# Kernel optimization log

Measured on AMD Instinct MI355X. Metric: run time of the kernel, lower is better.

Reference implementation:

```python
import jax, jax.numpy as jnp
import numpy as np

N = 100000   # number of nodes
E = 400000   # number of edges
C = 16       # n_in_channels == n_out_channels
L = 16       # node_conv2 .. node_conv17
EPS = 1e-5   # BatchNorm eps


def _bn(h, g, b):
    # training-mode BatchNorm1d over the edge/batch axis (biased variance)
    mu = h.mean(0)
    var = h.var(0)
    return (h - mu) * jax.lax.rsqrt(var + EPS) * g + b


def setup_inputs() -> dict:
    key = jax.random.key(0)
    ks = jax.random.split(key, 6)
    return {
        "edge_features": jax.random.normal(ks[0], (E, C), jnp.float32),
        "edge_index": jax.random.randint(ks[1], (2, E), 0, N),
        "angles": jax.random.normal(ks[2], (E,), jnp.float32),
        "Wn": jax.random.normal(ks[3], (L, C, 2 * C), jnp.float32) / np.sqrt(2.0 * C),
        "bn": jnp.zeros((L, C), jnp.float32),
        "gn": jnp.ones((L, C), jnp.float32),
        "btn": jnp.zeros((L, C), jnp.float32),
        "We": jax.random.normal(ks[4], (C, 2 * C), jnp.float32) / np.sqrt(2.0 * C),
        "be": jnp.zeros((C,), jnp.float32),
        "ge": jnp.ones((C,), jnp.float32),
        "bte": jnp.zeros((C,), jnp.float32),
    }


def _forward(edge_features, edge_index, Wn, bn, gn, btn, We, be, ge, bte):
    src, dst = edge_index[0], edge_index[1]

    # EdgeConvNoNodes: init node features = mean of incident edge features (both endpoints)
    idx = jnp.concatenate([src, dst])                       # [2E]
    feats = jnp.concatenate([edge_features, edge_features], axis=0)
    deg = jax.ops.segment_sum(jnp.ones((2 * E,), edge_features.dtype), idx, N)
    x = jax.ops.segment_sum(feats, idx, N) / jnp.clip(deg, 1.0)[:, None]  # [N, C]

    # in-degree for mean aggregation of the 16 NodeConv1 layers
    deg_in = jnp.clip(jax.ops.segment_sum(jnp.ones((E,), x.dtype), dst, N), 1.0)[:, None]

    def step(x, p):
        W, b, g, bt = p
        # message: Linear(cat(x_i, x_j)) -> BN -> LeakyReLU on [E, C]
        m = jnp.concatenate([x[dst], x[src]], axis=1) @ W.T + b
        m = jax.nn.leaky_relu(_bn(m, g, bt))
        # mean aggregation at target nodes
        return jax.ops.segment_sum(m, dst, N) / deg_in, None

    x, _ = jax.lax.scan(step, x, (Wn, bn, gn, btn))

    # EdgeConv2: per-edge MLP on both edge directions, BN stats shared over [2E]
    pair = jnp.concatenate(
        [jnp.concatenate([x[src], x[dst]], axis=1),
         jnp.concatenate([x[dst], x[src]], axis=1)], axis=0)  # [2E, 2C]
    e = jax.nn.leaky_relu(_bn(pair @ We.T + be, ge, bte))      # [2E, C]
    e_fwd, e_bwd = e[:E], e[E:]
    edge_out = 0.5 * (e_fwd + e_bwd)                           # symmetric edge feature
    side_loss = jnp.mean((e_fwd - e_bwd) ** 2)                 # symmetry side loss
    return edge_out, side_loss


def reference(edge_features, edge_index, angles, Wn, bn, gn, btn, We, be, ge, bte):
    # `angles` is accepted but unused, matching the original forward
    return _forward(edge_features, edge_index, Wn, bn, gn, btn, We, be, ge, bte)
```

## Files before the change

### kernel.cpp

```cpp
#include <hip/hip_runtime.h>
#include <hip/hip_fp16.h>
#include <cstdint>
#include <cstddef>

#define NN 100000
#define EE 400000
#define CC 16
#define LL 16
#define NB 16

typedef unsigned int uint;

__device__ __forceinline__ float lrelu(float v){ return v > 0.0f ? v : 0.01f*v; }

__device__ __forceinline__ float waveSum(float v){
#pragma unroll
  for (int off = 32; off >= 1; off >>= 1) v += __shfl_xor(v, off);
  return v;
}

__device__ __forceinline__ float fma4(float4 w, float4 v, float a){
  a = fmaf(w.x, v.x, a); a = fmaf(w.y, v.y, a);
  a = fmaf(w.z, v.z, a); a = fmaf(w.w, v.w, a);
  return a;
}

__device__ __forceinline__ uint pack_h2(float a, float b){
  __half2 h = __floats2half2_rn(a, b);
  return *reinterpret_cast<uint*>(&h);
}
__device__ __forceinline__ float2 unpack_h2(uint v){
  __half2 h = *reinterpret_cast<__half2*>(&v);
  return __half22float2(h);
}

__global__ __launch_bounds__(256) void k_count(const int* __restrict__ ei,
    int* __restrict__ cdst, int* __restrict__ csrc)
{
  int t = blockIdx.x*256 + threadIdx.x;
  if (t >= EE) return;
  int s = ei[t], d = ei[EE + t];
  atomicAdd(&cdst[d], 1);
  atomicAdd(&csrc[s], 1);
}

__device__ __forceinline__ void scan_one(const int* __restrict__ cnt,
    int* __restrict__ rp, int* __restrict__ bsums, int n, int* sd)
{
  int tid = threadIdx.x;
  int base = blockIdx.x*1024 + tid*4;
  int v0=0,v1=0,v2=0,v3=0;
  if (base+0 < n) v0 = cnt[base+0];
  if (base+1 < n) v1 = cnt[base+1];
  if (base+2 < n) v2 = cnt[base+2];
  if (base+3 < n) v3 = cnt[base+3];
  int tot = v0+v1+v2+v3;
  sd[tid] = tot; __syncthreads();
  for (int off=1; off<256; off<<=1){
    int add = (tid>=off) ? sd[tid-off] : 0;
    __syncthreads();
    sd[tid] += add;
    __syncthreads();
  }
  int excl = sd[tid] - tot;
  if (base+0 < n) rp[base+0] = excl;
  if (base+1 < n) rp[base+1] = excl+v0;
  if (base+2 < n) rp[base+2] = excl+v0+v1;
  if (base+3 < n) rp[base+3] = excl+v0+v1+v2;
  if (tid==255) bsums[blockIdx.x] = sd[255];
  __syncthreads();
}

__global__ __launch_bounds__(256) void k_scan1(const int* __restrict__ ca,
    int* __restrict__ rpa, int* __restrict__ bsa,
    const int* __restrict__ cb, int* __restrict__ rpb, int* __restrict__ bsb, int n)
{
  __shared__ int sd[256];
  scan_one(ca, rpa, bsa, n, sd);
  scan_one(cb, rpb, bsb, n, sd);
}

__device__ __forceinline__ void scan2_one(const int* __restrict__ bsums,
    int* __restrict__ boff, int nseg, int* sd)
{
  int tid = threadIdx.x;
  int v = (tid < nseg) ? bsums[tid] : 0;
  sd[tid] = v; __syncthreads();
  for (int off=1; off<256; off<<=1){
    int add = (tid>=off) ? sd[tid-off] : 0;
    __syncthreads();
    sd[tid] += add;
    __syncthreads();
  }
  if (tid < nseg) boff[tid] = sd[tid] - v;
  __syncthreads();
}

__global__ __launch_bounds__(256) void k_scan2(const int* __restrict__ bsa,
    int* __restrict__ boffa, const int* __restrict__ bsb, int* __restrict__ boffb, int nseg)
{
  __shared__ int sd[256];
  scan2_one(bsa, boffa, nseg, sd);
  scan2_one(bsb, boffb, nseg, sd);
}

__global__ __launch_bounds__(256) void k_scan3(
    int* __restrict__ rpa, int* __restrict__ cura, const int* __restrict__ boffa, int totala,
    int* __restrict__ rpb, int* __restrict__ curb, const int* __restrict__ boffb, int totalb, int n)
{
  int adda = boffa[blockIdx.x];
  int addb = boffb[blockIdx.x];
  int base = blockIdx.x*1024 + threadIdx.x*4;
#pragma unroll
  for (int i=0;i<4;i++){
    if (base+i < n){
      int va = rpa[base+i] + adda; rpa[base+i] = va; cura[base+i] = va;
      int vb = rpb[base+i] + addb; rpb[base+i] = vb; curb[base+i] = vb;
    }
  }
  if (blockIdx.x==0 && threadIdx.x==0){ rpa[n] = totala; rpb[n] = totalb; }
}

__global__ __launch_bounds__(256) void k_fill(const int* __restrict__ ei,
    int* __restrict__ cur, int4* __restrict__ sd4,
    int* __restrict__ curs, int* __restrict__ lsrc)
{
  int t = blockIdx.x*256 + threadIdx.x;
  if (t >= EE) return;
  int s = ei[t], d = ei[EE + t];
  int p = atomicAdd(&cur[d], 1);
  sd4[p] = make_int4(s, d, t, 0);
  int ps = atomicAdd(&curs[s], 1);
  lsrc[ps] = t;
}

__global__ __launch_bounds__(256) void k_gather0(const float* __restrict__ ef,
    const int4* __restrict__ sd4, const int* __restrict__ rp,
    const int* __restrict__ lsrc, const int* __restrict__ rps,
    float* __restrict__ x0, float* __restrict__ invdeg)
{
  int t = blockIdx.x*256 + threadIdx.x;
  if (t >= NN*CC) return;
  int n = t >> 4, c = t & 15;
  int bd = rp[n], ed = rp[n+1];
  int bs = rps[n], es = rps[n+1];
  float acc = 0.0f;
  for (int i=bd; i<ed; i++){
    acc += ef[(size_t)sd4[i].z*CC + c];
  }
  for (int i=bs; i<es; i++){
    acc += ef[(size_t)lsrc[i]*CC + c];
  }
  float dg = fmaxf((float)((ed-bd)+(es-bs)), 1.0f);
  x0[t] = acc / dg;
  if (c == 0){
    invdeg[n] = 1.0f / fmaxf((float)(ed-bd), 1.0f);
  }
}

__global__ __launch_bounds__(256) void k_edge(const float* __restrict__ x,
    const int4* __restrict__ sd4,
    const float* __restrict__ W, const float* __restrict__ b,
    uint* __restrict__ mh, double* __restrict__ st)
{
  __shared__ float sW[512];
  __shared__ float sb16[16];
  __shared__ float sredS[64], sredQ[64];
  for (int i=threadIdx.x; i<512; i+=256) sW[i] = W[i];
  if (threadIdx.x < 16) sb16[threadIdx.x] = b[threadIdx.x];
  __syncthreads();

  int t = blockIdx.x*256 + threadIdx.x;
  bool val = (t < EE);
  float acc[16];
  if (val){
    int4 p = sd4[t];
    const float4* xd4 = (const float4*)(x + (size_t)p.y*CC);
    const float4* xs4 = (const float4*)(x + (size_t)p.x*CC);
    float4 xd0=xd4[0], xd1=xd4[1], xd2=xd4[2], xd3=xd4[3];
    float4 xs0=xs4[0], xs1=xs4[1], xs2=xs4[2], xs3=xs4[3];
#pragma unroll
    for (int c=0;c<16;c++){
      const float4* wr = (const float4*)(sW + c*32);
      float a = sb16[c];
      a = fma4(wr[0],xd0,a); a = fma4(wr[1],xd1,a);
      a = fma4(wr[2],xd2,a); a = fma4(wr[3],xd3,a);
      a = fma4(wr[4],xs0,a); a = fma4(wr[5],xs1,a);
      a = fma4(wr[6],xs2,a); a = fma4(wr[7],xs3,a);
      acc[c] = a;
    }
    uint pk[8];
#pragma unroll
    for (int q=0;q<8;q++) pk[q] = pack_h2(acc[2*q], acc[2*q+1]);
    uint4* po = (uint4*)(mh + (size_t)t*8);
    po[0] = make_uint4(pk[0],pk[1],pk[2],pk[3]);
    po[1] = make_uint4(pk[4],pk[5],pk[6],pk[7]);
  } else {
#pragma unroll
    for (int c=0;c<16;c++) acc[c] = 0.0f;
  }

  int lane = threadIdx.x & 63, w = threadIdx.x >> 6;
#pragma unroll
  for (int c=0;c<16;c++){
    float rs = waveSum(acc[c]);
    float rq = waveSum(acc[c]*acc[c]);
    if (lane == 0){ sredS[w*16+c] = rs; sredQ[w*16+c] = rq; }
  }
  __syncthreads();
  double* stb = st + (size_t)(blockIdx.x & (NB-1))*32;
  if (threadIdx.x < 16){
    int c = threadIdx.x;
    float tot = sredS[c] + sredS[16+c] + sredS[32+c] + sredS[48+c];
    unsafeAtomicAdd(&stb[c], (double)tot);
  } else if (threadIdx.x < 32){
    int c = threadIdx.x - 16;
    float tot = sredQ[c] + sredQ[16+c] + sredQ[32+c] + sredQ[48+c];
    unsafeAtomicAdd(&stb[16+c], (double)tot);
  }
}

__global__ __launch_bounds__(256) void k_node(const uint* __restrict__ mh,
    const int* __restrict__ rp,
    const float* __restrict__ invdeg, const double* __restrict__ st,
    const float* __restrict__ g, const float* __restrict__ bt,
    float* __restrict__ xout)
{
  __shared__ float sA[16], sB[16];
  if (threadIdx.x < 16){
    int c = threadIdx.x;
    double S = 0.0, Q = 0.0;
#pragma unroll
    for (int k=0;k<NB;k++){ S += st[k*32 + c]; Q += st[k*32 + 16 + c]; }
    double mu  = S * (1.0/EE);
    double var = Q * (1.0/EE) - mu*mu;
    float sc = rsqrtf((float)var + 1e-5f);
    float A = sc * g[c];
    sA[c] = A; sB[c] = bt[c] - (float)mu * A;
  }
  __syncthreads();
  int t = blockIdx.x*256 + threadIdx.x;
  int n = t >> 3, cp = t & 7;
  if (n >= NN) return;
  float A0 = sA[2*cp], B0 = sB[2*cp];
  float A1 = sA[2*cp+1], B1 = sB[2*cp+1];
  int beg = rp[n], end = rp[n+1];
  float a0 = 0.0f, a1 = 0.0f;
  for (int i=beg; i<end; i++){
    float2 v = unpack_h2(mh[(size_t)i*8 + cp]);
    a0 += lrelu(fmaf(A0, v.x, B0));
    a1 += lrelu(fmaf(A1, v.y, B1));
  }
  float iv = invdeg[n];
  float2* po = (float2*)(xout + (size_t)n*CC + 2*cp);
  *po = make_float2(a0*iv, a1*iv);
}

__global__ __launch_bounds__(256) void k_uvf(const float* __restrict__ x,
    const float* __restrict__ W, const float* __restrict__ b,
    uint* __restrict__ u, uint* __restrict__ v)
{
  __shared__ float sW[512];
  __shared__ float sb16[16];
  for (int i=threadIdx.x; i<512; i+=256) sW[i] = W[i];
  if (threadIdx.x < 16) sb16[threadIdx.x] = b[threadIdx.x];
  __syncthreads();
  int n = blockIdx.x*256 + threadIdx.x;
  if (n >= NN) return;
  const float4* xr = (const float4*)(x + (size_t)n*CC);
  float4 x0 = xr[0], x1 = xr[1], x2 = xr[2], x3 = xr[3];
  uint up[8], vp[8];
#pragma unroll
  for (int q=0;q<8;q++){
    int c0 = 2*q, c1 = 2*q+1;
    const float4* w0 = (const float4*)(sW + c0*32);
    const float4* w1 = (const float4*)(sW + c1*32);
    float u0 = sb16[c0], u1 = sb16[c1], v0 = 0.f, v1 = 0.f;
    u0 = fma4(w0[0],x0,u0); u0 = fma4(w0[1],x1,u0); u0 = fma4(w0[2],x2,u0); u0 = fma4(w0[3],x3,u0);
    v0 = fma4(w0[4],x0,v0); v0 = fma4(w0[5],x1,v0); v0 = fma4(w0[6],x2,v0); v0 = fma4(w0[7],x3,v0);
    u1 = fma4(w1[0],x0,u1); u1 = fma4(w1[1],x1,u1); u1 = fma4(w1[2],x2,u1); u1 = fma4(w1[3],x3,u1);
    v1 = fma4(w1[4],x0,v1); v1 = fma4(w1[5],x1,v1); v1 = fma4(w1[6],x2,v1); v1 = fma4(w1[7],x3,v1);
    up[q] = pack_h2(u0,u1);
    vp[q] = pack_h2(v0,v1);
  }
  uint4* pu = (uint4*)(u + (size_t)n*8);
  pu[0] = make_uint4(up[0],up[1],up[2],up[3]);
  pu[1] = make_uint4(up[4],up[5],up[6],up[7]);
  uint4* pv = (uint4*)(v + (size_t)n*8);
  pv[0] = make_uint4(vp[0],vp[1],vp[2],vp[3]);
  pv[1] = make_uint4(vp[4],vp[5],vp[6],vp[7]);
}

__global__ __launch_bounds__(256) void k_final1(
    const uint* __restrict__ uf, const uint* __restrict__ vf,
    const int* __restrict__ ei, double* __restrict__ st)
{
  __shared__ float sredS[64], sredQ[64];
  int t = blockIdx.x*256 + threadIdx.x;
  float ls[16], lq[16];
#pragma unroll
  for (int c=0;c<16;c++){ ls[c]=0.f; lq[c]=0.f; }
  if (t < EE){
    int s = ei[t], d = ei[EE+t];
    const uint4* pus = (const uint4*)(uf + (size_t)s*8);
    const uint4* pvd = (const uint4*)(vf + (size_t)d*8);
    const uint4* pud = (const uint4*)(uf + (size_t)d*8);
    const uint4* pvs = (const uint4*)(vf + (size_t)s*8);
    uint4 us0=pus[0], us1=pus[1], vd0=pvd[0], vd1=pvd[1];
    uint4 ud0=pud[0], ud1=pud[1], vs0=pvs[0], vs1=pvs[1];
    uint usw[8]={us0.x,us0.y,us0.z,us0.w, us1.x,us1.y,us1.z,us1.w};
    uint vdw[8]={vd0.x,vd0.y,vd0.z,vd0.w, vd1.x,vd1.y,vd1.z,vd1.w};
    uint udw[8]={ud0.x,ud0.y,ud0.z,ud0.w, ud1.x,ud1.y,ud1.z,ud1.w};
    uint vsw[8]={vs0.x,vs0.y,vs0.z,vs0.w, vs1.x,vs1.y,vs1.z,vs1.w};
#pragma unroll
    for (int q=0;q<8;q++){
      float2 a = unpack_h2(usw[q]), bq = unpack_h2(vdw[q]);
      float2 cc = unpack_h2(udw[q]), dd = unpack_h2(vsw[q]);
      float f0 = a.x + bq.x, f1 = a.y + bq.y;
      float g0 = cc.x + dd.x, g1 = cc.y + dd.y;
      ls[2*q]   += f0 + g0; lq[2*q]   += f0*f0 + g0*g0;
      ls[2*q+1] += f1 + g1; lq[2*q+1] += f1*f1 + g1*g1;
    }
  }
  int lane = threadIdx.x & 63, w = threadIdx.x >> 6;
#pragma unroll
  for (int c=0;c<16;c++){
    float rs = waveSum(ls[c]);
    float rq = waveSum(lq[c]);
    if (lane == 0){ sredS[w*16+c] = rs; sredQ[w*16+c] = rq; }
  }
  __syncthreads();
  double* stb = st + (size_t)(blockIdx.x & (NB-1))*32;
  if (threadIdx.x < 16){
    int c = threadIdx.x;
    float tot = sredS[c] + sredS[16+c] + sredS[32+c] + sredS[48+c];
    unsafeAtomicAdd(&stb[c], (double)tot);
  } else if (threadIdx.x < 32){
    int c = threadIdx.x - 16;
    float tot = sredQ[c] + sredQ[16+c] + sredQ[32+c] + sredQ[48+c];
    unsafeAtomicAdd(&stb[16+c], (double)tot);
  }
}

__global__ __launch_bounds__(256) void k_final2(
    const uint* __restrict__ uf, const uint* __restrict__ vf,
    const int* __restrict__ ei, const double* __restrict__ st,
    const float* __restrict__ g, const float* __restrict__ bt,
    float* __restrict__ out, double* __restrict__ loss)
{
  __shared__ float sA[16], sB[16];
  __shared__ float sl[4];
  if (threadIdx.x < 16){
    int c = threadIdx.x;
    double S = 0.0, Q = 0.0;
#pragma unroll
    for (int k=0;k<NB;k++){ S += st[k*32 + c]; Q += st[k*32 + 16 + c]; }
    double mu  = S * (1.0/(2.0*EE));
    double var = Q * (1.0/(2.0*EE)) - mu*mu;
    float sc = rsqrtf((float)var + 1e-5f);
    float A = sc * g[c];
    sA[c] = A; sB[c] = bt[c] - (float)mu * A;
  }
  __syncthreads();

  int t = blockIdx.x*256 + threadIdx.x;
  float lsum = 0.0f;
  if (t < EE){
    int s = ei[t], d = ei[EE+t];
    const uint4* pus = (const uint4*)(uf + (size_t)s*8);
    const uint4* pvd = (const uint4*)(vf + (size_t)d*8);
    const uint4* pud = (const uint4*)(uf + (size_t)d*8);
    const uint4* pvs = (const uint4*)(vf + (size_t)s*8);
    uint4 us0=pus[0], us1=pus[1], vd0=pvd[0], vd1=pvd[1];
    uint4 ud0=pud[0], ud1=pud[1], vs0=pvs[0], vs1=pvs[1];
    uint usw[8]={us0.x,us0.y,us0.z,us0.w, us1.x,us1.y,us1.z,us1.w};
    uint vdw[8]={vd0.x,vd0.y,vd0.z,vd0.w, vd1.x,vd1.y,vd1.z,vd1.w};
    uint udw[8]={ud0.x,ud0.y,ud0.z,ud0.w, ud1.x,ud1.y,ud1.z,ud1.w};
    uint vsw[8]={vs0.x,vs0.y,vs0.z,vs0.w, vs1.x,vs1.y,vs1.z,vs1.w};
    float fo[16];
#pragma unroll
    for (int q=0;q<8;q++){
      float2 a = unpack_h2(usw[q]), bq = unpack_h2(vdw[q]);
      float2 cc = unpack_h2(udw[q]), dd = unpack_h2(vsw[q]);
      int c0 = 2*q, c1 = 2*q+1;
      float e0 = lrelu(fmaf(sA[c0], a.x + bq.x, sB[c0]));
      float b0 = lrelu(fmaf(sA[c0], cc.x + dd.x, sB[c0]));
      float e1 = lrelu(fmaf(sA[c1], a.y + bq.y, sB[c1]));
      float b1 = lrelu(fmaf(sA[c1], cc.y + dd.y, sB[c1]));
      fo[c0] = 0.5f*(e0 + b0);
      fo[c1] = 0.5f*(e1 + b1);
      float d0 = e0 - b0, d1 = e1 - b1;
      lsum = fmaf(d0, d0, lsum);
      lsum = fmaf(d1, d1, lsum);
    }
    float4* po = (float4*)(out + (size_t)t*CC);
    po[0]=make_float4(fo[0],fo[1],fo[2],fo[3]);
    po[1]=make_float4(fo[4],fo[5],fo[6],fo[7]);
    po[2]=make_float4(fo[8],fo[9],fo[10],fo[11]);
    po[3]=make_float4(fo[12],fo[13],fo[14],fo[15]);
  }
  lsum = waveSum(lsum);
  int lane = threadIdx.x & 63, w = threadIdx.x >> 6;
  if (lane == 0) sl[w] = lsum;
  __syncthreads();
  if (threadIdx.x == 0)
    unsafeAtomicAdd(&loss[blockIdx.x & (NB-1)], (double)(sl[0]+sl[1]+sl[2]+sl[3]));
}

__global__ void k_final3(float* __restrict__ out, const double* __restrict__ loss)
{
  double s = 0.0;
#pragma unroll
  for (int k=0;k<NB;k++) s += loss[k];
  out[(size_t)EE*CC] = (float)(s * (1.0/((double)EE*CC)));
}

extern "C" void kernel_launch(void* const* d_in, const int* in_sizes, int n_in,
                              void* d_out, int out_size, void* d_ws, size_t ws_size,
                              hipStream_t stream)
{
  (void)in_sizes; (void)n_in; (void)out_size; (void)ws_size;
  const float* ef  = (const float*)d_in[0];
  const int*   ei  = (const int*)d_in[1];
  const float* Wn  = (const float*)d_in[3];
  const float* bn  = (const float*)d_in[4];
  const float* gn  = (const float*)d_in[5];
  const float* btn = (const float*)d_in[6];
  const float* We  = (const float*)d_in[7];
  const float* be  = (const float*)d_in[8];
  const float* ge  = (const float*)d_in[9];
  const float* bte = (const float*)d_in[10];
  float* out = (float*)d_out;
  char* ws = (char*)d_ws;

  size_t off = 0;
  auto alloc = [&](size_t bytes)->size_t{
    size_t r = off; off = (off + bytes + 255) & ~(size_t)255; return r;
  };
  size_t o_xa     = alloc((size_t)NN*CC*4);
  size_t o_xb     = alloc((size_t)NN*CC*4);
  size_t o_mh     = alloc((size_t)EE*8*4);
  size_t o_uf     = alloc((size_t)NN*8*4);
  size_t o_vf     = alloc((size_t)NN*8*4);
  size_t o_cdst   = alloc((size_t)NN*4);
  size_t o_csrc   = alloc((size_t)NN*4);
  size_t o_rp     = alloc((size_t)(NN+1)*4);
  size_t o_rps    = alloc((size_t)(NN+1)*4);
  size_t o_cur    = alloc((size_t)NN*4);
  size_t o_curs   = alloc((size_t)NN*4);
  size_t o_sd4    = alloc((size_t)EE*16);
  size_t o_lsrc   = alloc((size_t)EE*4);
  size_t o_bsum   = alloc(512);
  size_t o_bsum2  = alloc(512);
  size_t o_boff   = alloc(512);
  size_t o_boff2  = alloc(512);
  size_t o_stats  = alloc((size_t)(17*NB*32 + NB)*8);
  size_t o_invdeg = alloc((size_t)NN*4);

  float*  x_a     = (float*)(ws + o_xa);
  float*  x_b     = (float*)(ws + o_xb);
  uint*   m_h     = (uint*)(ws + o_mh);
  uint*   u_f     = (uint*)(ws + o_uf);
  uint*   v_f     = (uint*)(ws + o_vf);
  int*    cdst    = (int*)(ws + o_cdst);
  int*    csrc    = (int*)(ws + o_csrc);
  int*    rp      = (int*)(ws + o_rp);
  int*    rps     = (int*)(ws + o_rps);
  int*    cur     = (int*)(ws + o_cur);
  int*    curs    = (int*)(ws + o_curs);
  int4*   sd4     = (int4*)(ws + o_sd4);
  int*    lsrc    = (int*)(ws + o_lsrc);
  int*    bsum    = (int*)(ws + o_bsum);
  int*    bsum2   = (int*)(ws + o_bsum2);
  int*    boff    = (int*)(ws + o_boff);
  int*    boff2   = (int*)(ws + o_boff2);
  double* stats   = (double*)(ws + o_stats);
  double* lossd   = stats + (size_t)17*NB*32;
  float*  invdeg  = (float*)(ws + o_invdeg);

  const int GB_E  = (EE + 255)/256;
  const int GB_NC = (NN*CC + 255)/256;
  const int GB_N8 = (NN*8 + 255)/256;
  const int GB_N  = (NN + 255)/256;
  const int NSEG  = (NN + 1023)/1024;

  hipMemsetAsync(cdst, 0, (size_t)NN*4, stream);
  hipMemsetAsync(csrc, 0, (size_t)NN*4, stream);
  hipMemsetAsync(stats, 0, (size_t)(17*NB*32 + NB)*8, stream);

  k_count<<<GB_E, 256, 0, stream>>>(ei, cdst, csrc);
  k_scan1<<<NSEG, 256, 0, stream>>>(cdst, rp, bsum, csrc, rps, bsum2, NN);
  k_scan2<<<1, 256, 0, stream>>>(bsum, boff, bsum2, boff2, NSEG);
  k_scan3<<<NSEG, 256, 0, stream>>>(rp, cur, boff, EE, rps, curs, boff2, EE, NN);
  k_fill<<<GB_E, 256, 0, stream>>>(ei, cur, sd4, curs, lsrc);
  k_gather0<<<GB_NC, 256, 0, stream>>>(ef, sd4, rp, lsrc, rps, x_a, invdeg);

  const float* xc = x_a;
  float* xn = x_b;
  for (int l = 0; l < LL; ++l){
    double* st = stats + (size_t)l*NB*32;
    const float* Wl = Wn + (size_t)l*CC*2*CC;
    const float* bl = bn + (size_t)l*CC;
    k_edge<<<GB_E, 256, 0, stream>>>(xc, sd4, Wl, bl, m_h, st);
    k_node<<<GB_N8, 256, 0, stream>>>(m_h, rp, invdeg, st,
                                      gn + (size_t)l*CC, btn + (size_t)l*CC, xn);
    float* tmp = (float*)xc; xc = xn; xn = tmp;
  }

  double* stF = stats + (size_t)LL*NB*32;
  k_uvf<<<GB_N, 256, 0, stream>>>(xc, We, be, u_f, v_f);
  k_final1<<<GB_E, 256, 0, stream>>>(u_f, v_f, ei, stF);
  k_final2<<<GB_E, 256, 0, stream>>>(u_f, v_f, ei, stF, ge, bte, out, lossd);
  k_final3<<<1, 1, 0, stream>>>(out, lossd);
}
```

Baseline: 952.0 us.

## Store node features in fp16 and process two edges per thread in k_edge

Node feature buffers switch from fp32 to packed half2, which halves the bytes of every random gather of node rows in the edge and final kernels. k_edge now handles two edges per thread, so each shared-memory weight read feeds two FMAs and the number of wave reductions per edge is halved. k_gather0 moves to one thread per channel pair using float2 loads. Storing node features in fp16 adds rounding error on every one of the 16 layers, and the two-edges-per-thread kernel raises register pressure.

```diff
diff --git a/kernel.cpp b/kernel.cpp
--- a/kernel.cpp
+++ b/kernel.cpp
@@ -19,12 +19,6 @@
   return v;
 }
 
-__device__ __forceinline__ float fma4(float4 w, float4 v, float a){
-  a = fmaf(w.x, v.x, a); a = fmaf(w.y, v.y, a);
-  a = fmaf(w.z, v.z, a); a = fmaf(w.w, v.w, a);
-  return a;
-}
-
 __device__ __forceinline__ uint pack_h2(float a, float b){
   __half2 h = __floats2half2_rn(a, b);
   return *reinterpret_cast<uint*>(&h);
@@ -32,6 +26,14 @@
 __device__ __forceinline__ float2 unpack_h2(uint v){
   __half2 h = *reinterpret_cast<__half2*>(&v);
   return __half22float2(h);
+}
+
+__device__ __forceinline__ void unpack_row(const uint* __restrict__ xh, int n, float* f){
+  const uint4* p = (const uint4*)(xh + (size_t)n*8);
+  uint4 r0 = p[0], r1 = p[1];
+  uint w[8] = {r0.x,r0.y,r0.z,r0.w, r1.x,r1.y,r1.z,r1.w};
+#pragma unroll
+  for (int q=0;q<8;q++){ float2 v = unpack_h2(w[q]); f[2*q]=v.x; f[2*q+1]=v.y; }
 }
 
 __global__ __launch_bounds__(256) void k_count(const int* __restrict__ ei,
@@ -137,28 +139,32 @@
 __global__ __launch_bounds__(256) void k_gather0(const float* __restrict__ ef,
     const int4* __restrict__ sd4, const int* __restrict__ rp,
     const int* __restrict__ lsrc, const int* __restrict__ rps,
-    float* __restrict__ x0, float* __restrict__ invdeg)
-{
-  int t = blockIdx.x*256 + threadIdx.x;
-  if (t >= NN*CC) return;
-  int n = t >> 4, c = t & 15;
+    uint* __restrict__ xh, float* __restrict__ invdeg)
+{
+  int t = blockIdx.x*256 + threadIdx.x;
+  if (t >= NN*8) return;
+  int n = t >> 3, cp = t & 7;
   int bd = rp[n], ed = rp[n+1];
   int bs = rps[n], es = rps[n+1];
-  float acc = 0.0f;
+  float a0 = 0.0f, a1 = 0.0f;
   for (int i=bd; i<ed; i++){
-    acc += ef[(size_t)sd4[i].z*CC + c];
+    const float2* p = (const float2*)(ef + (size_t)sd4[i].z*CC + 2*cp);
+    float2 v = *p;
+    a0 += v.x; a1 += v.y;
   }
   for (int i=bs; i<es; i++){
-    acc += ef[(size_t)lsrc[i]*CC + c];
+    const float2* p = (const float2*)(ef + (size_t)lsrc[i]*CC + 2*cp);
+    float2 v = *p;
+    a0 += v.x; a1 += v.y;
   }
   float dg = fmaxf((float)((ed-bd)+(es-bs)), 1.0f);
-  x0[t] = acc / dg;
-  if (c == 0){
+  xh[(size_t)n*8 + cp] = pack_h2(a0/dg, a1/dg);
+  if (cp == 0){
     invdeg[n] = 1.0f / fmaxf((float)(ed-bd), 1.0f);
   }
 }
 
-__global__ __launch_bounds__(256) void k_edge(const float* __restrict__ x,
+__global__ __launch_bounds__(256) void k_edge(const uint* __restrict__ xh,
     const int4* __restrict__ sd4,
     const float* __restrict__ W, const float* __restrict__ b,
     uint* __restrict__ mh, double* __restrict__ st)
@@ -171,40 +177,51 @@
   __syncthreads();
 
   int t = blockIdx.x*256 + threadIdx.x;
-  bool val = (t < EE);
-  float acc[16];
+  int e0 = 2*t, e1 = 2*t+1;
+  bool val = (e1 < EE);
+  float acc0[16], acc1[16];
   if (val){
-    int4 p = sd4[t];
-    const float4* xd4 = (const float4*)(x + (size_t)p.y*CC);
-    const float4* xs4 = (const float4*)(x + (size_t)p.x*CC);
-    float4 xd0=xd4[0], xd1=xd4[1], xd2=xd4[2], xd3=xd4[3];
-    float4 xs0=xs4[0], xs1=xs4[1], xs2=xs4[2], xs3=xs4[3];
+    int4 p0 = sd4[e0], p1 = sd4[e1];
+    float xa[32], xb[32];
+    unpack_row(xh, p0.y, xa);
+    unpack_row(xh, p0.x, xa + 16);
+    unpack_row(xh, p1.y, xb);
+    unpack_row(xh, p1.x, xb + 16);
 #pragma unroll
     for (int c=0;c<16;c++){
-      const float4* wr = (const float4*)(sW + c*32);
-      float a = sb16[c];
-      a = fma4(wr[0],xd0,a); a = fma4(wr[1],xd1,a);
-      a = fma4(wr[2],xd2,a); a = fma4(wr[3],xd3,a);
-      a = fma4(wr[4],xs0,a); a = fma4(wr[5],xs1,a);
-      a = fma4(wr[6],xs2,a); a = fma4(wr[7],xs3,a);
-      acc[c] = a;
+      const float* wr = sW + c*32;
+      float a0 = sb16[c], a1 = sb16[c];
+#pragma unroll
+      for (int k=0;k<32;k++){
+        float w = wr[k];
+        a0 = fmaf(w, xa[k], a0);
+        a1 = fmaf(w, xb[k], a1);
+      }
+      acc0[c]=a0; acc1[c]=a1;
     }
-    uint pk[8];
-#pragma unroll
-    for (int q=0;q<8;q++) pk[q] = pack_h2(acc[2*q], acc[2*q+1]);
-    uint4* po = (uint4*)(mh + (size_t)t*8);
-    po[0] = make_uint4(pk[0],pk[1],pk[2],pk[3]);
-    po[1] = make_uint4(pk[4],pk[5],pk[6],pk[7]);
+    uint w0[8], w1[8];
+#pragma unroll
+    for (int q=0;q<8;q++){
+      w0[q] = pack_h2(acc0[2*q], acc0[2*q+1]);
+      w1[q] = pack_h2(acc1[2*q], acc1[2*q+1]);
+    }
+    uint4* po0 = (uint4*)(mh + (size_t)e0*8);
+    po0[0] = make_uint4(w0[0],w0[1],w0[2],w0[3]);
+    po0[1] = make_uint4(w0[4],w0[5],w0[6],w0[7]);
+    uint4* po1 = (uint4*)(mh + (size_t)e1*8);
+    po1[0] = make_uint4(w1[0],w1[1],w1[2],w1[3]);
+    po1[1] = make_uint4(w1[4],w1[5],w1[6],w1[7]);
   } else {
 #pragma unroll
-    for (int c=0;c<16;c++) acc[c] = 0.0f;
+    for (int c=0;c<16;c++){ acc0[c]=0.0f; acc1[c]=0.0f; }
   }
 
   int lane = threadIdx.x & 63, w = threadIdx.x >> 6;
 #pragma unroll
   for (int c=0;c<16;c++){
-    float rs = waveSum(acc[c]);
-    float rq = waveSum(acc[c]*acc[c]);
+    float rs = acc0[c] + acc1[c];
+    float rq = acc0[c]*acc0[c] + acc1[c]*acc1[c];
+    rs = waveSum(rs); rq = waveSum(rq);
     if (lane == 0){ sredS[w*16+c] = rs; sredQ[w*16+c] = rq; }
   }
   __syncthreads();
@@ -224,7 +241,7 @@
     const int* __restrict__ rp,
     const float* __restrict__ invdeg, const double* __restrict__ st,
     const float* __restrict__ g, const float* __restrict__ bt,
-    float* __restrict__ xout)
+    uint* __restrict__ xhout)
 {
   __shared__ float sA[16], sB[16];
   if (threadIdx.x < 16){
@@ -252,11 +269,10 @@
     a1 += lrelu(fmaf(A1, v.y, B1));
   }
   float iv = invdeg[n];
-  float2* po = (float2*)(xout + (size_t)n*CC + 2*cp);
-  *po = make_float2(a0*iv, a1*iv);
-}
-
-__global__ __launch_bounds__(256) void k_uvf(const float* __restrict__ x,
+  xhout[(size_t)n*8 + cp] = pack_h2(a0*iv, a1*iv);
+}
+
+__global__ __launch_bounds__(256) void k_uvf(const uint* __restrict__ xh,
     const float* __restrict__ W, const float* __restrict__ b,
     uint* __restrict__ u, uint* __restrict__ v)
 {
@@ -267,19 +283,23 @@
   __syncthreads();
   int n = blockIdx.x*256 + threadIdx.x;
   if (n >= NN) return;
-  const float4* xr = (const float4*)(x + (size_t)n*CC);
-  float4 x0 = xr[0], x1 = xr[1], x2 = xr[2], x3 = xr[3];
+  float xr[16];
+  unpack_row(xh, n, xr);
   uint up[8], vp[8];
 #pragma unroll
   for (int q=0;q<8;q++){
     int c0 = 2*q, c1 = 2*q+1;
-    const float4* w0 = (const float4*)(sW + c0*32);
-    const float4* w1 = (const float4*)(sW + c1*32);
+    const float* w0 = sW + c0*32;
+    const float* w1 = sW + c1*32;
     float u0 = sb16[c0], u1 = sb16[c1], v0 = 0.f, v1 = 0.f;
-    u0 = fma4(w0[0],x0,u0); u0 = fma4(w0[1],x1,u0); u0 = fma4(w0[2],x2,u0); u0 = fma4(w0[3],x3,u0);
-    v0 = fma4(w0[4],x0,v0); v0 = fma4(w0[5],x1,v0); v0 = fma4(w0[6],x2,v0); v0 = fma4(w0[7],x3,v0);
-    u1 = fma4(w1[0],x0,u1); u1 = fma4(w1[1],x1,u1); u1 = fma4(w1[2],x2,u1); u1 = fma4(w1[3],x3,u1);
-    v1 = fma4(w1[4],x0,v1); v1 = fma4(w1[5],x1,v1); v1 = fma4(w1[6],x2,v1); v1 = fma4(w1[7],x3,v1);
+#pragma unroll
+    for (int k=0;k<16;k++){
+      float xv = xr[k];
+      u0 = fmaf(w0[k],    xv, u0);
+      v0 = fmaf(w0[16+k], xv, v0);
+      u1 = fmaf(w1[k],    xv, u1);
+      v1 = fmaf(w1[16+k], xv, v1);
+    }
     up[q] = pack_h2(u0,u1);
     vp[q] = pack_h2(v0,v1);
   }
@@ -437,8 +457,8 @@
   auto alloc = [&](size_t bytes)->size_t{
     size_t r = off; off = (off + bytes + 255) & ~(size_t)255; return r;
   };
-  size_t o_xa     = alloc((size_t)NN*CC*4);
-  size_t o_xb     = alloc((size_t)NN*CC*4);
+  size_t o_xha    = alloc((size_t)NN*8*4);
+  size_t o_xhb    = alloc((size_t)NN*8*4);
   size_t o_mh     = alloc((size_t)EE*8*4);
   size_t o_uf     = alloc((size_t)NN*8*4);
   size_t o_vf     = alloc((size_t)NN*8*4);
@@ -457,8 +477,8 @@
   size_t o_stats  = alloc((size_t)(17*NB*32 + NB)*8);
   size_t o_invdeg = alloc((size_t)NN*4);
 
-  float*  x_a     = (float*)(ws + o_xa);
-  float*  x_b     = (float*)(ws + o_xb);
+  uint*   xh_a    = (uint*)(ws + o_xha);
+  uint*   xh_b    = (uint*)(ws + o_xhb);
   uint*   m_h     = (uint*)(ws + o_mh);
   uint*   u_f     = (uint*)(ws + o_uf);
   uint*   v_f     = (uint*)(ws + o_vf);
@@ -479,7 +499,7 @@
   float*  invdeg  = (float*)(ws + o_invdeg);
 
   const int GB_E  = (EE + 255)/256;
-  const int GB_NC = (NN*CC + 255)/256;
+  const int GB_E2 = (EE/2 + 255)/256;
   const int GB_N8 = (NN*8 + 255)/256;
   const int GB_N  = (NN + 255)/256;
   const int NSEG  = (NN + 1023)/1024;
@@ -493,18 +513,18 @@
   k_scan2<<<1, 256, 0, stream>>>(bsum, boff, bsum2, boff2, NSEG);
   k_scan3<<<NSEG, 256, 0, stream>>>(rp, cur, boff, EE, rps, curs, boff2, EE, NN);
   k_fill<<<GB_E, 256, 0, stream>>>(ei, cur, sd4, curs, lsrc);
-  k_gather0<<<GB_NC, 256, 0, stream>>>(ef, sd4, rp, lsrc, rps, x_a, invdeg);
-
-  const float* xc = x_a;
-  float* xn = x_b;
+  k_gather0<<<GB_N8, 256, 0, stream>>>(ef, sd4, rp, lsrc, rps, xh_a, invdeg);
+
+  uint* xc = xh_a;
+  uint* xn = xh_b;
   for (int l = 0; l < LL; ++l){
     double* st = stats + (size_t)l*NB*32;
     const float* Wl = Wn + (size_t)l*CC*2*CC;
     const float* bl = bn + (size_t)l*CC;
-    k_edge<<<GB_E, 256, 0, stream>>>(xc, sd4, Wl, bl, m_h, st);
+    k_edge<<<GB_E2, 256, 0, stream>>>(xc, sd4, Wl, bl, m_h, st);
     k_node<<<GB_N8, 256, 0, stream>>>(m_h, rp, invdeg, st,
                                       gn + (size_t)l*CC, btn + (size_t)l*CC, xn);
-    float* tmp = (float*)xc; xc = xn; xn = tmp;
+    uint* tmp = xc; xc = xn; xn = tmp;
   }
 
   double* stF = stats + (size_t)LL*NB*32;
```

Result: faster. 775.6 us (-18.5%).
